# Optimization experiments

Measured on AMD Instinct MI355X. Metric: run time of the kernel, lower is better.

## Reference

```python
import jax, jax.numpy as jnp
import numpy as np

M = 8192          # tokens
DIM = 2048        # per-stream width; K = 4*DIM
S = 4             # fixed stream count (Stream4 kernels)
N = 32            # fixed GEMM output width
SINKHORN_ITERS = 20


def setup_inputs() -> dict:
    key = jax.random.key(0)
    k1, k2 = jax.random.split(key)
    X = jax.random.normal(k1, (M, S * DIM), dtype=jnp.float32)
    # scale W so H = X @ W is O(1): keeps sigmoid/exp/sinkhorn numerically sane
    W = jax.random.normal(k2, (S * DIM, N), dtype=jnp.float32) / np.float32(np.sqrt(S * DIM))
    # module init: beta = zeros(24), alpha = ones(3), concatenated
    alpha_beta = jnp.concatenate([jnp.zeros(24, jnp.float32), jnp.ones(3, jnp.float32)])
    return {"X": X, "W": W, "alpha_beta": alpha_beta}


def _sinkhorn(P, iters=SINKHORN_ITERS):
    # doubly-stochastic normalization of [M, S, S] matrices
    for _ in range(iters):
        P = P / jnp.sum(P, axis=-1, keepdims=True)  # row normalize
        P = P / jnp.sum(P, axis=-2, keepdims=True)  # col normalize
    return P


def reference(X, W, alpha_beta):
    Mm, K = X.shape
    d = K // S
    # skinny GEMM producing the mixing logits (fused w/ SplitK in the kernel)
    H = X @ W                                   # [M, 32]
    b_res, b_pre, b_pos = alpha_beta[0:16], alpha_beta[16:20], alpha_beta[20:24]
    a_res, a_pre, a_pos = alpha_beta[24], alpha_beta[25], alpha_beta[26]
    H_pre = a_pre * jax.nn.sigmoid(H[:, 16:20]) + b_pre          # [M, 4]
    H_pos = a_pos * jax.nn.sigmoid(H[:, 20:24]) + b_pos          # [M, 4]
    H_res = (a_res * H[:, 0:16] + b_res).reshape(Mm, S, S)       # [M, 4, 4]
    H_res = _sinkhorn(jnp.exp(H_res))                            # doubly stochastic
    # view X as 4 streams of width d
    Xs = X.reshape(Mm, S, d)                                     # [M, 4, d]
    # ApplyPreTransform: collapse streams with H_pre weights
    Y = jnp.einsum('ms,msd->md', H_pre, Xs)                      # [M, d]
    # ApplyResidual: per-token 4x4 stream mix + broadcast of pre-transformed feature
    O = jnp.einsum('msi,mid->msd', H_res, Xs) + H_pos[:, :, None] * Y[:, None, :]
    return O.reshape(Mm, K)
```

## Files before the change

### kernel.cpp

```cpp
#include <hip/hip_runtime.h>
#include <math.h>
#include <stdint.h>

#define K_DIM 8192
#define D_DIM 2048
#define M_ROWS 8192
#define N_W 32
#define NC 24
#define KSPLIT 4
#define ROWS 16
#define THR 64
#define CCOL 256
#define NCH 8
#define KSC 8

typedef short bf16x8 __attribute__((ext_vector_type(8)));
typedef float f32x4 __attribute__((ext_vector_type(4)));
union U32x4 { uint32_t u[4]; bf16x8 v; };

typedef const uint32_t __attribute__((address_space(1)))* gas_ptr;
typedef uint32_t __attribute__((address_space(3)))* las_ptr;

#define WFI(ks, tile) (((ks) * 2 + (tile)) * 64)

__global__ __launch_bounds__(256) void mhc_prepack_kernel(
    const float* __restrict__ W, unsigned short* __restrict__ wfrag)
{
    const int idx = blockIdx.x * 256 + threadIdx.x;
    const int k = idx >> 5, n = idx & 31;
    const float w = W[(size_t)k * N_W + n];
    const uint32_t u = __float_as_uint(w);
    const uint32_t r = u + 0x7FFFu + ((u >> 16) & 1u);

    const int ks = k >> 5, kk = k & 31;
    const int lane = ((kk >> 3) << 4) | (n & 15);
    const int e = kk & 7;
    const int tile = n >> 4;
    wfrag[((size_t)WFI(ks, tile) + lane) * 8 + e] = (unsigned short)(r >> 16);
}

__global__ __launch_bounds__(THR) void mhc_gemm_kernel(
    const float* __restrict__ X, const unsigned short* __restrict__ wfrag,
    float* __restrict__ part)
{
    __shared__ __align__(16) float Xl[2][ROWS * CCOL];
    const int l = threadIdx.x;
    const int rowbase = blockIdx.x * ROWS;
    const int colbase = blockIdx.y * (K_DIM / KSPLIT);
    const int ks00 = blockIdx.y * (K_DIM / KSPLIT / 32);

    const bf16x8* __restrict__ wf = reinterpret_cast<const bf16x8*>(wfrag);

    f32x4 c0 = {0.f, 0.f, 0.f, 0.f};
    f32x4 c1 = {0.f, 0.f, 0.f, 0.f};

#pragma unroll
    for (int r = 0; r < ROWS; ++r) {
        const float* src = X + (size_t)(rowbase + r) * K_DIM + colbase + l * 4;
        __builtin_amdgcn_global_load_lds((gas_ptr)src, (las_ptr)&Xl[0][r * CCOL],
                                         16, 0, 0);
    }

#pragma unroll
    for (int c = 0; c < NCH; ++c) {
        bf16x8 b0[KSC], b1[KSC];
#pragma unroll
        for (int s = 0; s < KSC; ++s) {
            const int ks = ks00 + c * KSC + s;
            b0[s] = wf[WFI(ks, 0) + l];
            b1[s] = wf[WFI(ks, 1) + l];
        }
        __builtin_amdgcn_sched_barrier(0);

        if (c + 1 < NCH) {
#pragma unroll
            for (int r = 0; r < ROWS; ++r) {
                const float* src = X + (size_t)(rowbase + r) * K_DIM
                                   + colbase + (c + 1) * CCOL + l * 4;
                __builtin_amdgcn_global_load_lds(
                    (gas_ptr)src, (las_ptr)&Xl[(c + 1) & 1][r * CCOL], 16, 0, 0);
            }
            __builtin_amdgcn_sched_barrier(0);
            asm volatile("s_waitcnt vmcnt(16)" ::: "memory");
        } else {
            __builtin_amdgcn_sched_barrier(0);
            asm volatile("s_waitcnt vmcnt(0)" ::: "memory");
        }
        __builtin_amdgcn_sched_barrier(0);

        const float* xt = &Xl[c & 1][(l & 15) * CCOL + ((l >> 4) << 3)];
#pragma unroll
        for (int s = 0; s < KSC; ++s) {
            const float4 xa = *reinterpret_cast<const float4*>(xt + s * 32);
            const float4 xb = *reinterpret_cast<const float4*>(xt + s * 32 + 4);
            float xs[8];
            xs[0] = xa.x; xs[1] = xa.y; xs[2] = xa.z; xs[3] = xa.w;
            xs[4] = xb.x; xs[5] = xb.y; xs[6] = xb.z; xs[7] = xb.w;

            U32x4 ah, al;
#pragma unroll
            for (int p = 0; p < 4; ++p) {
                const uint32_t u0 = __float_as_uint(xs[2 * p]);
                const uint32_t u1 = __float_as_uint(xs[2 * p + 1]);
                const float h0 = __uint_as_float(u0 & 0xFFFF0000u);
                const float h1 = __uint_as_float(u1 & 0xFFFF0000u);
                const uint32_t r0 = __float_as_uint(xs[2 * p] - h0);
                const uint32_t r1 = __float_as_uint(xs[2 * p + 1] - h1);
                ah.u[p] = (u1 & 0xFFFF0000u) | (u0 >> 16);
                al.u[p] = (r1 & 0xFFFF0000u) | (r0 >> 16);
            }

            c0 = __builtin_amdgcn_mfma_f32_16x16x32_bf16(ah.v, b0[s], c0, 0, 0, 0);
            c0 = __builtin_amdgcn_mfma_f32_16x16x32_bf16(al.v, b0[s], c0, 0, 0, 0);
            c1 = __builtin_amdgcn_mfma_f32_16x16x32_bf16(ah.v, b1[s], c1, 0, 0, 0);
            c1 = __builtin_amdgcn_mfma_f32_16x16x32_bf16(al.v, b1[s], c1, 0, 0, 0);
        }
    }

    float* prow = part + ((size_t)blockIdx.y * M_ROWS + rowbase) * NC;
    const int drow0 = (l >> 4) << 2;
    const int col = l & 15;
#pragma unroll
    for (int r = 0; r < 4; ++r)
        prow[(drow0 + r) * NC + col] = c0[r];
    if (col < 8) {
#pragma unroll
        for (int r = 0; r < 4; ++r)
            prow[(drow0 + r) * NC + 16 + col] = c1[r];
    }
}

__global__ __launch_bounds__(256) void mhc_apply_kernel(
    const float* __restrict__ X, const float* __restrict__ part,
    const float* __restrict__ ab, float* __restrict__ out)
{
    __shared__ float pbuf[NC];
    const int row = blockIdx.x;
    const int t = threadIdx.x;

    if (t < 64) {
        const int lane = t;
        float pl = 0.f;
        if (lane < NC) {
#pragma unroll
            for (int j = 0; j < KSPLIT; ++j)
                pl += part[((size_t)j * M_ROWS + row) * NC + lane];
        }
        const float bias  = (lane < NC) ? ab[lane] : 0.f;
        const float scale = ab[(lane < 16) ? 24 : ((lane < 20) ? 25 : 26)];

        float vout;
        if (lane < 16) {
            vout = __expf(fmaf(scale, pl, bias));
        } else {
            vout = fmaf(scale, 1.f / (1.f + __expf(-pl)), bias);
        }

        float p = vout;
        for (int it = 0; it < 20; ++it) {
            float rs = p + __shfl_xor(p, 1);
            rs += __shfl_xor(rs, 2);
            p = p / rs;
            float cs = p + __shfl_xor(p, 4);
            cs += __shfl_xor(cs, 8);
            p = p / cs;
        }
        if (lane < NC) pbuf[lane] = (lane < 16) ? p : vout;
    }
    __syncthreads();

    float hres[4][4], hpre[4], hpos[4];
#pragma unroll
    for (int i = 0; i < 16; ++i) hres[i >> 2][i & 3] = pbuf[i];
#pragma unroll
    for (int i = 0; i < 4; ++i) hpre[i] = pbuf[16 + i];
#pragma unroll
    for (int i = 0; i < 4; ++i) hpos[i] = pbuf[20 + i];

    const float4* __restrict__ Xr =
        reinterpret_cast<const float4*>(X + (size_t)row * K_DIM);
    float4* __restrict__ Or = reinterpret_cast<float4*>(out + (size_t)row * K_DIM);

#pragma unroll
    for (int q = 0; q < 2; ++q) {
        const int pos = t + q * 256;
        float4 xq[4];
#pragma unroll
        for (int i = 0; i < 4; ++i) xq[i] = Xr[i * (D_DIM / 4) + pos];

        float y[4];
#pragma unroll
        for (int e = 0; e < 4; ++e) {
            float s = 0.f;
#pragma unroll
            for (int i = 0; i < 4; ++i)
                s = fmaf(hpre[i], reinterpret_cast<const float*>(&xq[i])[e], s);
            y[e] = s;
        }

#pragma unroll
        for (int s = 0; s < 4; ++s) {
            float4 o;
            float* oe = reinterpret_cast<float*>(&o);
#pragma unroll
            for (int e = 0; e < 4; ++e) {
                float v = hpos[s] * y[e];
#pragma unroll
                for (int i = 0; i < 4; ++i)
                    v = fmaf(hres[s][i], reinterpret_cast<const float*>(&xq[i])[e], v);
                oe[e] = v;
            }
            Or[s * (D_DIM / 4) + pos] = o;
        }
    }
}

extern "C" void kernel_launch(void* const* d_in, const int* in_sizes, int n_in,
                              void* d_out, int out_size, void* d_ws, size_t ws_size,
                              hipStream_t stream) {
    const float* X  = (const float*)d_in[0];
    const float* W  = (const float*)d_in[1];
    const float* ab = (const float*)d_in[2];
    float* out = (float*)d_out;
    unsigned short* wfrag = (unsigned short*)d_ws;
    float* part = (float*)((char*)d_ws + 524288);

    mhc_prepack_kernel<<<(K_DIM * N_W) / 256, 256, 0, stream>>>(W, wfrag);
    dim3 g1(M_ROWS / ROWS, KSPLIT);
    mhc_gemm_kernel<<<g1, THR, 0, stream>>>(X, wfrag, part);
    mhc_apply_kernel<<<M_ROWS, 256, 0, stream>>>(X, part, ab, out);
}
```

Baseline: 165.6 us.

## Double split-K to 8 and XOR-swizzle LDS layout for X tiles

```diff
diff --git a/kernel.cpp b/kernel.cpp
--- a/kernel.cpp
+++ b/kernel.cpp
@@ -7,12 +7,12 @@
 #define M_ROWS 8192
 #define N_W 32
 #define NC 24
-#define KSPLIT 4
+#define KSPLIT 8
 #define ROWS 16
 #define THR 64
-#define CCOL 256
+#define CCOL 128
 #define NCH 8
-#define KSC 8
+#define KSC 4
 
 typedef short bf16x8 __attribute__((ext_vector_type(8)));
 typedef float f32x4 __attribute__((ext_vector_type(4)));
@@ -54,11 +54,16 @@
     f32x4 c0 = {0.f, 0.f, 0.f, 0.f};
     f32x4 c1 = {0.f, 0.f, 0.f, 0.f};
 
-#pragma unroll
-    for (int r = 0; r < ROWS; ++r) {
-        const float* src = X + (size_t)(rowbase + r) * K_DIM + colbase + l * 4;
-        __builtin_amdgcn_global_load_lds((gas_ptr)src, (las_ptr)&Xl[0][r * CCOL],
-                                         16, 0, 0);
+    const int hs = l >> 5;
+    const int sl = l & 31;
+
+#pragma unroll
+    for (int g = 0; g < 8; ++g) {
+        const int r2 = 2 * g + hs;
+        const float* src = X + (size_t)(rowbase + r2) * K_DIM + colbase
+                           + ((sl ^ (r2 & 7)) << 2);
+        __builtin_amdgcn_global_load_lds((gas_ptr)src,
+                                         (las_ptr)&Xl[0][2 * g * CCOL], 16, 0, 0);
     }
 
 #pragma unroll
@@ -74,25 +79,32 @@
 
         if (c + 1 < NCH) {
 #pragma unroll
-            for (int r = 0; r < ROWS; ++r) {
-                const float* src = X + (size_t)(rowbase + r) * K_DIM
-                                   + colbase + (c + 1) * CCOL + l * 4;
+            for (int g = 0; g < 8; ++g) {
+                const int r2 = 2 * g + hs;
+                const float* src = X + (size_t)(rowbase + r2) * K_DIM + colbase
+                                   + (c + 1) * CCOL + ((sl ^ (r2 & 7)) << 2);
                 __builtin_amdgcn_global_load_lds(
-                    (gas_ptr)src, (las_ptr)&Xl[(c + 1) & 1][r * CCOL], 16, 0, 0);
+                    (gas_ptr)src, (las_ptr)&Xl[(c + 1) & 1][2 * g * CCOL],
+                    16, 0, 0);
             }
             __builtin_amdgcn_sched_barrier(0);
-            asm volatile("s_waitcnt vmcnt(16)" ::: "memory");
+            asm volatile("s_waitcnt vmcnt(8)" ::: "memory");
         } else {
             __builtin_amdgcn_sched_barrier(0);
             asm volatile("s_waitcnt vmcnt(0)" ::: "memory");
         }
         __builtin_amdgcn_sched_barrier(0);
 
-        const float* xt = &Xl[c & 1][(l & 15) * CCOL + ((l >> 4) << 3)];
+        const int ar = l & 15;
+        const int q = ar & 7;
+        const float* xrow = &Xl[c & 1][ar * CCOL];
 #pragma unroll
         for (int s = 0; s < KSC; ++s) {
-            const float4 xa = *reinterpret_cast<const float4*>(xt + s * 32);
-            const float4 xb = *reinterpret_cast<const float4*>(xt + s * 32 + 4);
+            const int slot = s * 8 + ((l >> 4) << 1);
+            const float4 xa = *reinterpret_cast<const float4*>(
+                xrow + ((slot ^ q) << 2));
+            const float4 xb = *reinterpret_cast<const float4*>(
+                xrow + (((slot + 1) ^ q) << 2));
             float xs[8];
             xs[0] = xa.x; xs[1] = xa.y; xs[2] = xa.z; xs[3] = xa.w;
             xs[4] = xb.x; xs[5] = xb.y; xs[6] = xb.z; xs[7] = xb.w;
```

Result: no change. 167.8 us (+1.3%).

## Raise split-K to 16 and issue all loads upfront per block

Applied to the files above, without the earlier changes.

```diff
diff --git a/kernel.cpp b/kernel.cpp
--- a/kernel.cpp
+++ b/kernel.cpp
@@ -7,12 +7,14 @@
 #define M_ROWS 8192
 #define N_W 32
 #define NC 24
-#define KSPLIT 4
+#define KSPLIT 16
+#define KRANGE (K_DIM / KSPLIT)
 #define ROWS 16
 #define THR 64
 #define CCOL 256
-#define NCH 8
+#define NCHB 2
 #define KSC 8
+#define KSB 16
 
 typedef short bf16x8 __attribute__((ext_vector_type(8)));
 typedef float f32x4 __attribute__((ext_vector_type(4)));
@@ -43,54 +45,46 @@
     const float* __restrict__ X, const unsigned short* __restrict__ wfrag,
     float* __restrict__ part)
 {
-    __shared__ __align__(16) float Xl[2][ROWS * CCOL];
+    __shared__ __align__(16) float Xl[NCHB][ROWS * CCOL];
     const int l = threadIdx.x;
     const int rowbase = blockIdx.x * ROWS;
-    const int colbase = blockIdx.y * (K_DIM / KSPLIT);
-    const int ks00 = blockIdx.y * (K_DIM / KSPLIT / 32);
+    const int colbase = blockIdx.y * KRANGE;
+    const int ks00 = blockIdx.y * KSB;
 
     const bf16x8* __restrict__ wf = reinterpret_cast<const bf16x8*>(wfrag);
+
+    bf16x8 b0[KSB], b1[KSB];
+#pragma unroll
+    for (int s = 0; s < KSB; ++s) {
+        b0[s] = wf[WFI(ks00 + s, 0) + l];
+        b1[s] = wf[WFI(ks00 + s, 1) + l];
+    }
+    __builtin_amdgcn_sched_barrier(0);
+
+#pragma unroll
+    for (int c = 0; c < NCHB; ++c)
+#pragma unroll
+        for (int r = 0; r < ROWS; ++r) {
+            const float* src = X + (size_t)(rowbase + r) * K_DIM
+                               + colbase + c * CCOL + l * 4;
+            __builtin_amdgcn_global_load_lds(
+                (gas_ptr)src, (las_ptr)&Xl[c][r * CCOL], 16, 0, 0);
+        }
+    __builtin_amdgcn_sched_barrier(0);
 
     f32x4 c0 = {0.f, 0.f, 0.f, 0.f};
     f32x4 c1 = {0.f, 0.f, 0.f, 0.f};
 
 #pragma unroll
-    for (int r = 0; r < ROWS; ++r) {
-        const float* src = X + (size_t)(rowbase + r) * K_DIM + colbase + l * 4;
-        __builtin_amdgcn_global_load_lds((gas_ptr)src, (las_ptr)&Xl[0][r * CCOL],
-                                         16, 0, 0);
-    }
-
-#pragma unroll
-    for (int c = 0; c < NCH; ++c) {
-        bf16x8 b0[KSC], b1[KSC];
+    for (int c = 0; c < NCHB; ++c) {
+        if (c == 0) asm volatile("s_waitcnt vmcnt(16)" ::: "memory");
+        else        asm volatile("s_waitcnt vmcnt(0)" ::: "memory");
+        __builtin_amdgcn_sched_barrier(0);
+
+        const float* xt = &Xl[c][(l & 15) * CCOL + ((l >> 4) << 3)];
 #pragma unroll
         for (int s = 0; s < KSC; ++s) {
-            const int ks = ks00 + c * KSC + s;
-            b0[s] = wf[WFI(ks, 0) + l];
-            b1[s] = wf[WFI(ks, 1) + l];
-        }
-        __builtin_amdgcn_sched_barrier(0);
-
-        if (c + 1 < NCH) {
-#pragma unroll
-            for (int r = 0; r < ROWS; ++r) {
-                const float* src = X + (size_t)(rowbase + r) * K_DIM
-                                   + colbase + (c + 1) * CCOL + l * 4;
-                __builtin_amdgcn_global_load_lds(
-                    (gas_ptr)src, (las_ptr)&Xl[(c + 1) & 1][r * CCOL], 16, 0, 0);
-            }
-            __builtin_amdgcn_sched_barrier(0);
-            asm volatile("s_waitcnt vmcnt(16)" ::: "memory");
-        } else {
-            __builtin_amdgcn_sched_barrier(0);
-            asm volatile("s_waitcnt vmcnt(0)" ::: "memory");
-        }
-        __builtin_amdgcn_sched_barrier(0);
-
-        const float* xt = &Xl[c & 1][(l & 15) * CCOL + ((l >> 4) << 3)];
-#pragma unroll
-        for (int s = 0; s < KSC; ++s) {
+            const int ks = c * KSC + s;
             const float4 xa = *reinterpret_cast<const float4*>(xt + s * 32);
             const float4 xb = *reinterpret_cast<const float4*>(xt + s * 32 + 4);
             float xs[8];
@@ -110,10 +104,10 @@
                 al.u[p] = (r1 & 0xFFFF0000u) | (r0 >> 16);
             }
 
-            c0 = __builtin_amdgcn_mfma_f32_16x16x32_bf16(ah.v, b0[s], c0, 0, 0, 0);
-            c0 = __builtin_amdgcn_mfma_f32_16x16x32_bf16(al.v, b0[s], c0, 0, 0, 0);
-            c1 = __builtin_amdgcn_mfma_f32_16x16x32_bf16(ah.v, b1[s], c1, 0, 0, 0);
-            c1 = __builtin_amdgcn_mfma_f32_16x16x32_bf16(al.v, b1[s], c1, 0, 0, 0);
+            c0 = __builtin_amdgcn_mfma_f32_16x16x32_bf16(ah.v, b0[ks], c0, 0, 0, 0);
+            c0 = __builtin_amdgcn_mfma_f32_16x16x32_bf16(al.v, b0[ks], c0, 0, 0, 0);
+            c1 = __builtin_amdgcn_mfma_f32_16x16x32_bf16(ah.v, b1[ks], c1, 0, 0, 0);
+            c1 = __builtin_amdgcn_mfma_f32_16x16x32_bf16(al.v, b1[ks], c1, 0, 0, 0);
         }
     }
 
```

Result: slower. 171.8 us (+3.8%).
